# Optimization experiments

Measured on AMD Instinct MI355X. Metric: run time of the kernel, lower is better.

The kernel has to match this reference:

```python
import jax, jax.numpy as jnp
import numpy as np

NUM_NODES = 20000
HIDDEN = 64
NUM_EDGES = 640000
LEAK = 0.2  # PyG GATConv negative_slope default


def gat_conv(x, w, a_src, a_dst, b, src, dst, n):
    # x: [N, F_in]; w: [F_in, H*C]; a_src/a_dst: [H, C]; edges j=src -> i=dst
    H, C = a_src.shape
    xe = (x @ w).reshape(n, H, C)                         # [N, H, C]
    es = jnp.einsum('nhc,hc->nh', xe, a_src)              # alpha_src per node
    ed = jnp.einsum('nhc,hc->nh', xe, a_dst)              # alpha_dst per node
    e = jax.nn.leaky_relu(es[src] + ed[dst], LEAK)        # [E, H] edge logits
    # segment softmax over each destination's incoming edges
    m = jax.ops.segment_max(e, dst, num_segments=n)
    p = jnp.exp(e - m[dst])
    s = jax.ops.segment_sum(p, dst, num_segments=n)
    alpha = p / s[dst]                                    # [E, H]
    out = jax.ops.segment_sum(alpha[:, :, None] * xe[src], dst, num_segments=n)
    return out.reshape(n, H * C) + b                      # concat heads + bias


def setup_inputs() -> dict:
    key = jax.random.key(0)
    ks = jax.random.split(key, 16)
    B, S, N, Hd = 4, 12, NUM_NODES, HIDDEN
    sc = 0.1
    inp = {}
    inp['x'] = jax.random.normal(ks[0], (B, S, N), jnp.float32)
    inp['edge_index'] = jax.random.randint(ks[1], (2, NUM_EDGES), 0, N, jnp.int32)
    inp['proj_w'] = jax.random.normal(ks[2], (S, Hd), jnp.float32) * sc
    inp['proj_b'] = jnp.zeros((Hd,), jnp.float32)
    inp['gat0_w'] = jax.random.normal(ks[3], (Hd, Hd), jnp.float32) * sc
    inp['gat0_asrc'] = jax.random.normal(ks[4], (8, 8), jnp.float32) * sc
    inp['gat0_adst'] = jax.random.normal(ks[5], (8, 8), jnp.float32) * sc
    inp['gat0_b'] = jnp.zeros((Hd,), jnp.float32)
    inp['gat1_w'] = jax.random.normal(ks[6], (Hd, Hd), jnp.float32) * sc
    inp['gat1_asrc'] = jax.random.normal(ks[7], (8, 8), jnp.float32) * sc
    inp['gat1_adst'] = jax.random.normal(ks[8], (8, 8), jnp.float32) * sc
    inp['gat1_b'] = jnp.zeros((Hd,), jnp.float32)
    inp['gat2_w'] = jax.random.normal(ks[9], (Hd, Hd), jnp.float32) * sc
    inp['gat2_asrc'] = jax.random.normal(ks[10], (1, Hd), jnp.float32) * sc
    inp['gat2_adst'] = jax.random.normal(ks[11], (1, Hd), jnp.float32) * sc
    inp['gat2_b'] = jnp.zeros((Hd,), jnp.float32)
    inp['conv_w'] = jax.random.normal(ks[12], (Hd, Hd, 3), jnp.float32) * sc
    inp['conv_b'] = jnp.zeros((Hd,), jnp.float32)
    inp['out_w'] = jax.random.normal(ks[13], (Hd, 3), jnp.float32) * sc
    inp['out_b'] = jnp.zeros((3,), jnp.float32)
    return inp


def reference(x, edge_index, proj_w, proj_b,
              gat0_w, gat0_asrc, gat0_adst, gat0_b,
              gat1_w, gat1_asrc, gat1_adst, gat1_b,
              gat2_w, gat2_asrc, gat2_adst, gat2_b,
              conv_w, conv_b, out_w, out_b):
    B, S, N = x.shape
    # PyG GATConv add_self_loops=True
    loops = jnp.arange(N, dtype=edge_index.dtype)
    src = jnp.concatenate([edge_index[0], loops])
    dst = jnp.concatenate([edge_index[1], loops])
    h = jnp.transpose(x, (0, 2, 1)) @ proj_w + proj_b     # [B, N, Hd]
    layers = [(gat0_w, gat0_asrc, gat0_adst, gat0_b),
              (gat1_w, gat1_asrc, gat1_adst, gat1_b),
              (gat2_w, gat2_asrc, gat2_adst, gat2_b)]
    for i, (w, asr, ads, b) in enumerate(layers):
        h = jax.vmap(lambda hb: gat_conv(hb, w, asr, ads, b, src, dst, N))(h)
        if i < len(layers) - 1:
            h = jax.nn.elu(h)                             # dropout is identity in eval
    hc = jnp.transpose(h, (0, 2, 1))                      # [B, Hd, N]
    hc = jax.lax.conv_general_dilated(hc, conv_w, (1,), ((1, 1),),
                                      dimension_numbers=('NCH', 'OIH', 'NCH'))
    hc = jax.nn.relu(hc + conv_b[None, :, None])
    h = jnp.transpose(hc, (0, 2, 1)) @ out_w + out_b      # [B, N, pred]
    return jnp.transpose(h, (0, 2, 1))                    # [B, pred, N]
```

## Files before the change

kernel.cpp:

```cpp
#include <hip/hip_runtime.h>
#include <math.h>

constexpr int B  = 4;
constexpr int S  = 12;
constexpr int N  = 20000;
constexpr int HD = 64;
constexpr int E0 = 640000;
constexpr int EL = E0 + N;
constexpr int BN = B * N;
constexpr int CAP = 128;

__global__ void scatter_kernel(const int* __restrict__ ei, int* __restrict__ cnt,
                               int* __restrict__ perm) {
    int e = blockIdx.x * blockDim.x + threadIdx.x;
    if (e >= EL) return;
    int s, d;
    if (e < E0) { s = ei[e]; d = ei[E0 + e]; }
    else        { s = e - E0; d = s; }
    int pos = atomicAdd(&cnt[d], 1) & (CAP - 1);
    perm[d * CAP + pos] = s;
}

__global__ void tw_kernel(const float* __restrict__ cw, float* __restrict__ cwD) {
    int i = blockIdx.x * blockDim.x + threadIdx.x;
    if (i >= HD * HD * 3) return;
    int o = i / (HD * 3), rem = i % (HD * 3), c = rem / 3, dt = rem % 3;
    cwD[dt * (HD * HD) + c * HD + o] = cw[i];
}

constexpr int GT = 64;

template<int H>
__global__ __launch_bounds__(256, 4)
void gemm_attn_kernel(const float* __restrict__ hin, const float* __restrict__ w,
                      const float* __restrict__ asrc, const float* __restrict__ adst,
                      float* __restrict__ xe, float* __restrict__ es, float* __restrict__ ed) {
    __shared__ float tile[GT * HD];
    int base = blockIdx.x * GT;
    for (int i = threadIdx.x; i < GT * (HD / 4); i += 256)
        ((float4*)tile)[i] = ((const float4*)(hin + (size_t)base * HD))[i];
    int lane = threadIdx.x & 63;
    float wres[HD];
    #pragma unroll
    for (int c = 0; c < HD; ++c) wres[c] = w[c * HD + lane];
    float as_ = asrc[lane], ad_ = adst[lane];
    __syncthreads();
    int wvid = threadIdx.x >> 6;
    for (int j = wvid * 16; j < wvid * 16 + 16; ++j) {
        int t = base + j;
        float acc = 0.f;
        #pragma unroll
        for (int cq = 0; cq < 16; ++cq) {
            float4 r = ((const float4*)tile)[j * 16 + cq];
            acc = fmaf(r.x, wres[4 * cq + 0], acc);
            acc = fmaf(r.y, wres[4 * cq + 1], acc);
            acc = fmaf(r.z, wres[4 * cq + 2], acc);
            acc = fmaf(r.w, wres[4 * cq + 3], acc);
        }
        xe[(size_t)t * HD + lane] = acc;
        float t0 = acc * as_, t1 = acc * ad_;
        if (H == 8) {
            #pragma unroll
            for (int m = 1; m < 8; m <<= 1) {
                t0 += __shfl_xor(t0, m, 64);
                t1 += __shfl_xor(t1, m, 64);
            }
            if ((lane & 7) == 0) {
                es[t * 8 + (lane >> 3)] = t0;
                ed[t * 8 + (lane >> 3)] = t1;
            }
        } else {
            #pragma unroll
            for (int m = 1; m < 64; m <<= 1) {
                t0 += __shfl_xor(t0, m, 64);
                t1 += __shfl_xor(t1, m, 64);
            }
            if (lane == 0) { es[t] = t0; ed[t] = t1; }
        }
    }
}

__global__ __launch_bounds__(256, 4)
void fused0_kernel(const float* __restrict__ x, const float* __restrict__ pw,
                   const float* __restrict__ pb, const float* __restrict__ w,
                   const float* __restrict__ asrc, const float* __restrict__ adst,
                   float* __restrict__ xe, float* __restrict__ es, float* __restrict__ ed) {
    __shared__ float tile[GT * HD];
    __shared__ float xt[S * GT];
    int base = blockIdx.x * GT;
    for (int i = threadIdx.x; i < S * GT; i += 256) {
        int s = i >> 6, nl = i & 63;
        int t = base + nl, bb = t / N, n = t - bb * N;
        xt[i] = x[(bb * S + s) * N + n];
    }
    int lane = threadIdx.x & 63;
    float wres[HD];
    #pragma unroll
    for (int c = 0; c < HD; ++c) wres[c] = w[c * HD + lane];
    float pwres[S];
    #pragma unroll
    for (int s = 0; s < S; ++s) pwres[s] = pw[s * HD + lane];
    float pbv = pb[lane];
    float as_ = asrc[lane], ad_ = adst[lane];
    __syncthreads();
    int wvid = threadIdx.x >> 6;
    for (int j = wvid * 16; j < wvid * 16 + 16; ++j) {
        float hl = pbv;
        #pragma unroll
        for (int s = 0; s < S; ++s)
            hl = fmaf(xt[s * GT + j], pwres[s], hl);
        tile[j * HD + lane] = hl;
    }
    for (int j = wvid * 16; j < wvid * 16 + 16; ++j) {
        int t = base + j;
        float acc = 0.f;
        #pragma unroll
        for (int cq = 0; cq < 16; ++cq) {
            float4 r = ((const float4*)tile)[j * 16 + cq];
            acc = fmaf(r.x, wres[4 * cq + 0], acc);
            acc = fmaf(r.y, wres[4 * cq + 1], acc);
            acc = fmaf(r.z, wres[4 * cq + 2], acc);
            acc = fmaf(r.w, wres[4 * cq + 3], acc);
        }
        xe[(size_t)t * HD + lane] = acc;
        float t0 = acc * as_, t1 = acc * ad_;
        #pragma unroll
        for (int m = 1; m < 8; m <<= 1) {
            t0 += __shfl_xor(t0, m, 64);
            t1 += __shfl_xor(t1, m, 64);
        }
        if ((lane & 7) == 0) {
            es[t * 8 + (lane >> 3)] = t0;
            ed[t * 8 + (lane >> 3)] = t1;
        }
    }
}

template<int H, bool DO_ELU>
__global__ __launch_bounds__(256, 8)
void agg_kernel(const float* __restrict__ xe, const float* __restrict__ es,
                const float* __restrict__ ed, const int* __restrict__ cnt,
                const int* __restrict__ perm, const float* __restrict__ bias,
                float* __restrict__ hout) {
    int g = blockIdx.x;
    int bb   = (g & 7) >> 1;
    int idx  = (g >> 3) * 2 + (g & 1);
    int node = idx * 4 + (threadIdx.x >> 6);
    int lane  = threadIdx.x & 63;
    int group = lane >> 4;
    int c4    = lane & 15;
    int deg = cnt[node];
    int baseE = node * CAP;
    int h = (H == 8) ? (c4 >> 1) : 0;
    const float*  es_b = es + bb * (N * H);
    const float4* xe4  = (const float4*)(xe + bb * (N * HD));
    float edv = ed[(bb * N + node) * H + h];
    float4 acc = {0.f, 0.f, 0.f, 0.f};
    float ssum = 0.f;
    #pragma unroll 4
    for (int jb = 0; jb < deg; jb += 4) {
        int j = jb + group;
        bool valid = (j < deg);
        int src = perm[baseE + (valid ? j : 0)];
        float e = es_b[src * H + h] + edv;
        e = fmaxf(e, 0.2f * e);
        float p = valid ? __expf(e) : 0.f;
        ssum += p;
        float4 xv = xe4[src * 16 + c4];
        acc.x = fmaf(p, xv.x, acc.x);
        acc.y = fmaf(p, xv.y, acc.y);
        acc.z = fmaf(p, xv.z, acc.z);
        acc.w = fmaf(p, xv.w, acc.w);
    }
    #pragma unroll
    for (int m = 16; m < 64; m <<= 1) {
        acc.x += __shfl_xor(acc.x, m, 64);
        acc.y += __shfl_xor(acc.y, m, 64);
        acc.z += __shfl_xor(acc.z, m, 64);
        acc.w += __shfl_xor(acc.w, m, 64);
        ssum  += __shfl_xor(ssum,  m, 64);
    }
    if (lane < 16) {
        float inv = 1.f / ssum;
        const float4* b4 = (const float4*)bias;
        float4 bv = b4[c4];
        float4 r;
        r.x = acc.x * inv + bv.x;
        r.y = acc.y * inv + bv.y;
        r.z = acc.z * inv + bv.z;
        r.w = acc.w * inv + bv.w;
        if (DO_ELU) {
            r.x = (r.x > 0.f) ? r.x : expm1f(r.x);
            r.y = (r.y > 0.f) ? r.y : expm1f(r.y);
            r.z = (r.z > 0.f) ? r.z : expm1f(r.z);
            r.w = (r.w > 0.f) ? r.w : expm1f(r.w);
        }
        ((float4*)hout)[(bb * N + node) * 16 + c4] = r;
    }
}

constexpr int CV2 = 16;
__global__ __launch_bounds__(128, 4)
void conv_out_kernel(const float* __restrict__ h, const float* __restrict__ cwD,
                     const float* __restrict__ cb, const float* __restrict__ ow,
                     const float* __restrict__ ob, float* __restrict__ out) {
    __shared__ alignas(16) float tile[(CV2 + 2) * HD];
    int bb = blockIdx.y;
    int base = blockIdx.x * CV2;
    const float4* hb4 = (const float4*)(h + (size_t)bb * N * HD);
    for (int i = threadIdx.x; i < (CV2 + 2) * (HD / 4); i += 128) {
        int r = i >> 4;
        int m = base + r - 1;
        float4 v = make_float4(0.f, 0.f, 0.f, 0.f);
        if (m >= 0 && m < N) v = hb4[(size_t)m * 16 + (i & 15)];
        ((float4*)tile)[i] = v;
    }
    int lane = threadIdx.x & 63;
    int wvid = threadIdx.x >> 6;
    float cbv = cb[lane];
    float ow0 = ow[lane * 3 + 0], ow1 = ow[lane * 3 + 1], ow2 = ow[lane * 3 + 2];
    float ob0 = ob[0], ob1 = ob[1], ob2 = ob[2];
    float acc[8];
    #pragma unroll
    for (int j = 0; j < 8; ++j) acc[j] = cbv;
    __syncthreads();
    #pragma unroll 1
    for (int dt = 0; dt < 3; ++dt) {
        #pragma unroll 1
        for (int ch = 0; ch < 2; ++ch) {
            float wres[32];
            #pragma unroll
            for (int c = 0; c < 32; ++c)
                wres[c] = cwD[dt * (HD * HD) + (ch * 32 + c) * HD + lane];
            #pragma unroll
            for (int j = 0; j < 8; ++j) {
                const float4* row =
                    (const float4*)(tile + (wvid * 8 + j + dt) * HD + ch * 32);
                float a = 0.f;
                #pragma unroll
                for (int cq = 0; cq < 8; ++cq) {
                    float4 r = row[cq];
                    a = fmaf(r.x, wres[4 * cq + 0], a);
                    a = fmaf(r.y, wres[4 * cq + 1], a);
                    a = fmaf(r.z, wres[4 * cq + 2], a);
                    a = fmaf(r.w, wres[4 * cq + 3], a);
                }
                acc[j] += a;
            }
        }
    }
    #pragma unroll
    for (int j = 0; j < 8; ++j) {
        float v = fmaxf(acc[j], 0.f);
        float t0 = v * ow0, t1 = v * ow1, t2 = v * ow2;
        #pragma unroll
        for (int m = 1; m < 64; m <<= 1) {
            t0 += __shfl_xor(t0, m, 64);
            t1 += __shfl_xor(t1, m, 64);
            t2 += __shfl_xor(t2, m, 64);
        }
        int n = base + wvid * 8 + j;
        if (lane < 3) {
            float r = (lane == 0) ? t0 + ob0 : (lane == 1) ? t1 + ob1 : t2 + ob2;
            out[(size_t)bb * 3 * N + lane * N + n] = r;
        }
    }
}

extern "C" void kernel_launch(void* const* d_in, const int* in_sizes, int n_in,
                              void* d_out, int out_size, void* d_ws, size_t ws_size,
                              hipStream_t stream) {
    const float* x      = (const float*)d_in[0];
    const int*   ei     = (const int*)  d_in[1];
    const float* proj_w = (const float*)d_in[2];
    const float* proj_b = (const float*)d_in[3];
    const float* g_w [3] = {(const float*)d_in[4], (const float*)d_in[8],  (const float*)d_in[12]};
    const float* g_as[3] = {(const float*)d_in[5], (const float*)d_in[9],  (const float*)d_in[13]};
    const float* g_ad[3] = {(const float*)d_in[6], (const float*)d_in[10], (const float*)d_in[14]};
    const float* g_b [3] = {(const float*)d_in[7], (const float*)d_in[11], (const float*)d_in[15]};
    const float* conv_w = (const float*)d_in[16];
    const float* conv_b = (const float*)d_in[17];
    const float* out_w  = (const float*)d_in[18];
    const float* out_b  = (const float*)d_in[19];
    float* out = (float*)d_out;

    float* bufA = (float*)d_ws;
    float* bufX = bufA + (size_t)BN * HD;
    float* es   = bufX + (size_t)BN * HD;
    float* ed   = es   + (size_t)BN * 8;
    int* cnt  = (int*)(ed + (size_t)BN * 8);
    int* perm = cnt + N;
    float* cwD = (float*)(perm + (size_t)N * CAP);

    const int TB = 256;
    const int gE = (EL + TB - 1) / TB;

    hipMemsetAsync(cnt, 0, N * sizeof(int), stream);
    scatter_kernel<<<gE, TB, 0, stream>>>(ei, cnt, perm);

    tw_kernel<<<(HD * HD * 3 + TB - 1) / TB, TB, 0, stream>>>(conv_w, cwD);

    fused0_kernel<<<BN / GT, TB, 0, stream>>>(x, proj_w, proj_b, g_w[0], g_as[0], g_ad[0],
                                              bufX, es, ed);
    agg_kernel<8, true><<<BN / 4, TB, 0, stream>>>(bufX, es, ed, cnt, perm, g_b[0], bufA);

    gemm_attn_kernel<8><<<BN / GT, TB, 0, stream>>>(bufA, g_w[1], g_as[1], g_ad[1], bufX, es, ed);
    agg_kernel<8, true><<<BN / 4, TB, 0, stream>>>(bufX, es, ed, cnt, perm, g_b[1], bufA);

    gemm_attn_kernel<1><<<BN / GT, TB, 0, stream>>>(bufA, g_w[2], g_as[2], g_ad[2], bufX, es, ed);
    agg_kernel<1, false><<<BN / 4, TB, 0, stream>>>(bufX, es, ed, cnt, perm, g_b[2], bufA);

    conv_out_kernel<<<dim3(N / CV2, B), 128, 0, stream>>>(bufA, cwD, conv_b, out_w, out_b, out);
}
```

Baseline: 456.3 us.

## Restructure conv_out to reuse tile rows across all three taps

The conv+output kernel now holds all three tap weight slices in registers. Each LDS row is read once and feeds up to three accumulators, instead of being reread once per tap. Blocks grow to 256 threads covering 40 nodes, so each wave produces 10 nodes. The final 64->3 projection is no longer a per-node wave-wide shuffle reduction: ReLU activations are staged in padded shared memory and 120 threads each compute one output dot product. This raises register pressure (about 96 weight registers) and leaves most threads idle during the output phase.

After: 1.061 ms. +132.5%, slower.

```diff
diff --git a/kernel.cpp b/kernel.cpp
--- a/kernel.cpp
+++ b/kernel.cpp
@@ -199,16 +199,16 @@
     }
 }
 
-constexpr int CV2 = 16;
-__global__ __launch_bounds__(128, 4)
+constexpr int CVN3 = 40;
+__global__ __launch_bounds__(256, 3)
 void conv_out_kernel(const float* __restrict__ h, const float* __restrict__ cwD,
                      const float* __restrict__ cb, const float* __restrict__ ow,
                      const float* __restrict__ ob, float* __restrict__ out) {
-    __shared__ alignas(16) float tile[(CV2 + 2) * HD];
+    __shared__ alignas(16) float tile[CVN3 * 68];
     int bb = blockIdx.y;
-    int base = blockIdx.x * CV2;
+    int base = blockIdx.x * CVN3;
     const float4* hb4 = (const float4*)(h + (size_t)bb * N * HD);
-    for (int i = threadIdx.x; i < (CV2 + 2) * (HD / 4); i += 128) {
+    for (int i = threadIdx.x; i < (CVN3 + 2) * (HD / 4); i += 256) {
         int r = i >> 4;
         int m = base + r - 1;
         float4 v = make_float4(0.f, 0.f, 0.f, 0.f);
@@ -217,53 +217,70 @@
     }
     int lane = threadIdx.x & 63;
     int wvid = threadIdx.x >> 6;
-    float cbv = cb[lane];
-    float ow0 = ow[lane * 3 + 0], ow1 = ow[lane * 3 + 1], ow2 = ow[lane * 3 + 2];
-    float ob0 = ob[0], ob1 = ob[1], ob2 = ob[2];
-    float acc[8];
-    #pragma unroll
-    for (int j = 0; j < 8; ++j) acc[j] = cbv;
+    float acc[10];
+    {
+        float cbv = cb[lane];
+        #pragma unroll
+        for (int j = 0; j < 10; ++j) acc[j] = cbv;
+    }
     __syncthreads();
     #pragma unroll 1
-    for (int dt = 0; dt < 3; ++dt) {
-        #pragma unroll 1
-        for (int ch = 0; ch < 2; ++ch) {
-            float wres[32];
+    for (int ch = 0; ch < 2; ++ch) {
+        float w0[32], w1[32], w2[32];
+        #pragma unroll
+        for (int c = 0; c < 32; ++c) {
+            w0[c] = cwD[0 * (HD * HD) + (ch * 32 + c) * HD + lane];
+            w1[c] = cwD[1 * (HD * HD) + (ch * 32 + c) * HD + lane];
+            w2[c] = cwD[2 * (HD * HD) + (ch * 32 + c) * HD + lane];
+        }
+        #pragma unroll
+        for (int rr = 0; rr < 12; ++rr) {
+            const float4* row =
+                (const float4*)(tile + (wvid * 10 + rr) * HD + ch * 32);
             #pragma unroll
-            for (int c = 0; c < 32; ++c)
-                wres[c] = cwD[dt * (HD * HD) + (ch * 32 + c) * HD + lane];
-            #pragma unroll
-            for (int j = 0; j < 8; ++j) {
-                const float4* row =
-                    (const float4*)(tile + (wvid * 8 + j + dt) * HD + ch * 32);
-                float a = 0.f;
-                #pragma unroll
-                for (int cq = 0; cq < 8; ++cq) {
-                    float4 r = row[cq];
-                    a = fmaf(r.x, wres[4 * cq + 0], a);
-                    a = fmaf(r.y, wres[4 * cq + 1], a);
-                    a = fmaf(r.z, wres[4 * cq + 2], a);
-                    a = fmaf(r.w, wres[4 * cq + 3], a);
+            for (int q = 0; q < 8; ++q) {
+                float4 r4 = row[q];
+                if (rr <= 9) {
+                    acc[rr] = fmaf(r4.x, w0[4*q+0], acc[rr]);
+                    acc[rr] = fmaf(r4.y, w0[4*q+1], acc[rr]);
+                    acc[rr] = fmaf(r4.z, w0[4*q+2], acc[rr]);
+                    acc[rr] = fmaf(r4.w, w0[4*q+3], acc[rr]);
                 }
-                acc[j] += a;
+                if (rr >= 1 && rr <= 10) {
+                    acc[rr-1] = fmaf(r4.x, w1[4*q+0], acc[rr-1]);
+                    acc[rr-1] = fmaf(r4.y, w1[4*q+1], acc[rr-1]);
+                    acc[rr-1] = fmaf(r4.z, w1[4*q+2], acc[rr-1]);
+                    acc[rr-1] = fmaf(r4.w, w1[4*q+3], acc[rr-1]);
+                }
+                if (rr >= 2) {
+                    acc[rr-2] = fmaf(r4.x, w2[4*q+0], acc[rr-2]);
+                    acc[rr-2] = fmaf(r4.y, w2[4*q+1], acc[rr-2]);
+                    acc[rr-2] = fmaf(r4.z, w2[4*q+2], acc[rr-2]);
+                    acc[rr-2] = fmaf(r4.w, w2[4*q+3], acc[rr-2]);
+                }
             }
         }
     }
-    #pragma unroll
-    for (int j = 0; j < 8; ++j) {
-        float v = fmaxf(acc[j], 0.f);
-        float t0 = v * ow0, t1 = v * ow1, t2 = v * ow2;
-        #pragma unroll
-        for (int m = 1; m < 64; m <<= 1) {
-            t0 += __shfl_xor(t0, m, 64);
-            t1 += __shfl_xor(t1, m, 64);
-            t2 += __shfl_xor(t2, m, 64);
-        }
-        int n = base + wvid * 8 + j;
-        if (lane < 3) {
-            float r = (lane == 0) ? t0 + ob0 : (lane == 1) ? t1 + ob1 : t2 + ob2;
-            out[(size_t)bb * 3 * N + lane * N + n] = r;
-        }
+    __syncthreads();
+    #pragma unroll
+    for (int j = 0; j < 10; ++j) {
+        int nl = wvid * 10 + j;
+        tile[nl * 68 + lane] = fmaxf(acc[j], 0.f);
+    }
+    __syncthreads();
+    if (wvid < 3 && lane < CVN3) {
+        int o = wvid;
+        float a = ob[o];
+        const float4* prow = (const float4*)(tile + lane * 68);
+        #pragma unroll
+        for (int q = 0; q < 16; ++q) {
+            float4 r4 = prow[q];
+            a = fmaf(r4.x, ow[(4*q+0) * 3 + o], a);
+            a = fmaf(r4.y, ow[(4*q+1) * 3 + o], a);
+            a = fmaf(r4.z, ow[(4*q+2) * 3 + o], a);
+            a = fmaf(r4.w, ow[(4*q+3) * 3 + o], a);
+        }
+        out[(size_t)bb * 3 * N + o * N + base + lane] = a;
     }
 }
 
@@ -310,5 +327,5 @@
     gemm_attn_kernel<1><<<BN / GT, TB, 0, stream>>>(bufA, g_w[2], g_as[2], g_ad[2], bufX, es, ed);
     agg_kernel<1, false><<<BN / 4, TB, 0, stream>>>(bufX, es, ed, cnt, perm, g_b[2], bufA);
 
-    conv_out_kernel<<<dim3(N / CV2, B), 128, 0, stream>>>(bufA, cwD, conv_b, out_w, out_b, out);
-}
+    conv_out_kernel<<<dim3(N / CVN3, B), TB, 0, stream>>>(bufA, cwD, conv_b, out_w, out_b, out);
+}
```
